# Optimization experiments

Measured on AMD Instinct MI355X. Metric: run time of the kernel, lower is better.

## Reference

```python
import jax, jax.numpy as jnp
import numpy as np

B, N, DIM = 2, 512, 128
HEADS, DH = 4, 64
INNER = HEADS * DH            # 256
POS_HID = 64
MULT = 4                      # attn_mlp_hidden_mult
K = 16                        # num_neighbors


def setup_inputs() -> dict:
    key = jax.random.key(0)
    ks = jax.random.split(key, 10)
    w = lambda k, shape: jax.random.normal(k, shape, jnp.float32) * 0.02
    return {
        "x": jax.random.normal(ks[0], (B, N, DIM), jnp.float32),
        "pos": jax.random.normal(ks[1], (B, N, 3), jnp.float32),
        "mask": jnp.ones((B, N), dtype=bool),
        "w_qkv": w(ks[2], (DIM, 3 * INNER)),
        "w_out": w(ks[3], (INNER, DIM)),
        "b_out": jnp.zeros((DIM,), jnp.float32),
        "w_pos1": w(ks[4], (3, POS_HID)),
        "b_pos1": jnp.zeros((POS_HID,), jnp.float32),
        "w_pos2": w(ks[5], (POS_HID, INNER)),
        "b_pos2": jnp.zeros((INNER,), jnp.float32),
        # grouped 1x1 convs == per-head linear layers
        "w_attn1": w(ks[6], (HEADS, DH, MULT * DH)),
        "b_attn1": jnp.zeros((HEADS, MULT * DH), jnp.float32),
        "w_attn2": w(ks[7], (HEADS, MULT * DH, DH)),
        "b_attn2": jnp.zeros((HEADS, DH), jnp.float32),
    }


def reference(x, pos, mask, w_qkv, w_out, b_out, w_pos1, b_pos1, w_pos2, b_pos2,
              w_attn1, b_attn1, w_attn2, b_attn2):
    b, n, _ = x.shape
    h, d = HEADS, DH

    qkv = x @ w_qkv                                   # [b, n, 3*inner]
    q, k, v = jnp.split(qkv, 3, axis=-1)
    to_heads = lambda t: t.reshape(b, n, h, d).transpose(0, 2, 1, 3)  # b h n d
    q, k, v = map(to_heads, (q, k, v))

    # dense pairwise relative positions + pos MLP  [b, n, n, inner]
    rel_pos = pos[:, :, None, :] - pos[:, None, :, :]            # [b, n, n, 3]
    rpe = jax.nn.relu(rel_pos @ w_pos1 + b_pos1) @ w_pos2 + b_pos2

    # masked topk over pairwise distance (smallest K)
    rel_dist = jnp.linalg.norm(rel_pos, axis=-1)                 # [b, n, n]
    mask2 = mask[:, :, None] & mask[:, None, :]                  # [b, n, n]
    fmax = jnp.finfo(rel_dist.dtype).max
    rel_dist = jnp.where(mask2, rel_dist, fmax)
    _, idx = jax.lax.top_k(-rel_dist, K)                         # [b, n, K]

    # neighbor gathers (equivalent to torch batched_index_select over j)
    gather_hd = jax.vmap(lambda t, i: t[:, i, :])                # [h,n,d],[n,K] -> [h,n,K,d]
    k_nb = gather_hd(k, idx)                                     # [b, h, n, K, d]
    v_nb = gather_hd(v, idx)
    row = jnp.arange(n)[:, None]
    rpe_nb = jax.vmap(lambda r, i: r[row, i])(rpe, idx)          # [b, n, K, inner]
    rpe_nb = rpe_nb.reshape(b, n, K, h, d).transpose(0, 3, 1, 2, 4)  # [b,h,n,K,d]
    mask_nb = jax.vmap(lambda m, i: m[row, i])(mask2, idx)       # [b, n, K]

    # qk_rel gathered implicitly: (q_i - k_j)[j=idx] == q_i - k_nb
    attn_in = q[:, :, :, None, :] - k_nb + rpe_nb                # [b, h, n, K, d]

    # grouped 1x1 conv MLP == per-head MLP on last dim
    hid = jax.nn.relu(jnp.einsum('bhikd,hde->bhike', attn_in, w_attn1)
                      + b_attn1[None, :, None, None, :])
    sim = (jnp.einsum('bhike,hed->bhikd', hid, w_attn2)
           + b_attn2[None, :, None, None, :])                    # [b, h, n, K, d]

    sim = jnp.where(mask_nb[:, None, :, :, None], sim, -fmax)
    # torch: sim is [b, (h d), i, j]; softmax(dim=-2) is over i -> axis 2 here
    attn = jax.nn.softmax(sim, axis=2)

    v_full = v_nb + rpe_nb                                       # [b, h, n, K, d]
    agg = jnp.sum(attn * v_full, axis=3)                         # [b, h, n, d]
    agg = agg.transpose(0, 2, 1, 3).reshape(b, n, h * d)         # [b, n, inner]
    return agg @ w_out + b_out
```

## Files before the change

### kernel.cpp

```cpp
#include <hip/hip_runtime.h>

#define B_ 2
#define N_ 512
#define DIM_ 128
#define HEADS_ 4
#define DH_ 64
#define INNER_ 256
#define PH_ 64
#define HID2_ 256
#define KNB_ 16

typedef unsigned long long u64;
typedef unsigned int u32;
typedef unsigned short u16;
typedef __attribute__((ext_vector_type(8))) short bf16x8;
typedef __attribute__((ext_vector_type(8))) unsigned short us8;
typedef __attribute__((ext_vector_type(4))) float f32x4;

__device__ __forceinline__ float bf2f(u16 u) {
    union { float f; u32 u; } c; c.u = ((u32)u) << 16; return c.f;
}
__device__ __forceinline__ u16 f2bf(float f) {
    union { float f; u32 u; } c; c.f = f;
    u32 u = c.u;
    return (u16)((u + 0x7fffu + ((u >> 16) & 1u)) >> 16);
}
__device__ __forceinline__ u32 pack2(float lo, float hi) {
    return ((u32)f2bf(hi) << 16) | (u32)f2bf(lo);
}

__global__ __launch_bounds__(256) void k_front(
        const float* __restrict__ x, const float* __restrict__ pos, const float* __restrict__ w_qkv,
        const float* __restrict__ w_a1, const float* __restrict__ w_a2, const float* __restrict__ w_p2,
        u16* __restrict__ wf1, u16* __restrict__ wf2, u16* __restrict__ wfp,
        u16* __restrict__ qb, u16* __restrict__ kb, float* __restrict__ v,
        int* __restrict__ idx) {
    int blk = blockIdx.x;
    if (blk < 576) {
        int t = blk * 256 + threadIdx.x;
        if (t < 65536) {
            int jj = t & 7, lbig = (t >> 3) & 63, f = t >> 9;
            int s = f & 1, etL = (f >> 1) & 7, half = (f >> 4) & 1, h = f >> 5;
            int lr = lbig & 15, g = lbig >> 4;
            int d = s * 32 + g * 8 + jj, e = (half * 8 + etL) * 16 + lr;
            wf1[t] = f2bf(w_a1[((h * 64 + d) << 8) + e]);
        } else if (t < 131072) {
            int t2 = t - 65536;
            int jj = t2 & 7, lbig = (t2 >> 3) & 63, f = t2 >> 9;
            int s = f & 7, ct = (f >> 3) & 3, h = f >> 5;
            int lr = lbig & 15, g = lbig >> 4;
            int e = s * 32 + g * 8 + jj, c = ct * 16 + lr;
            wf2[t2] = f2bf(w_a2[(((h << 8) + e) << 6) + c]);
        } else {
            int t3 = t - 131072;
            int jj = t3 & 7, lbig = (t3 >> 3) & 63, f = t3 >> 9;
            int s = f & 1, ct = (f >> 1) & 3, h = f >> 3;
            int lr = lbig & 15, g = lbig >> 4;
            int e = s * 32 + g * 8 + jj, c = h * 64 + ct * 16 + lr;
            wfp[t3] = f2bf(w_p2[(e << 8) + c]);
        }
    } else if (blk < 704) {
        int bu = blk - 576;
        int b = bu >> 6;
        int n0 = (bu & 63) * 8;
        int t = threadIdx.x;
        __shared__ float xs[8][128];
        #pragma unroll
        for (int p = 0; p < 4; ++p) {
            int e = p * 256 + t;
            xs[e >> 7][e & 127] = x[((size_t)(b * N_ + n0) + (e >> 7)) * DIM_ + (e & 127)];
        }
        __syncthreads();
        float acc[3][8];
        #pragma unroll
        for (int cc = 0; cc < 3; ++cc)
            #pragma unroll
            for (int r = 0; r < 8; ++r) acc[cc][r] = 0.f;
        for (int c4 = 0; c4 < 32; ++c4) {
            float wv[3][4];
            #pragma unroll
            for (int dd = 0; dd < 4; ++dd)
                #pragma unroll
                for (int cc = 0; cc < 3; ++cc)
                    wv[cc][dd] = w_qkv[(size_t)(c4 * 4 + dd) * (3 * INNER_) + cc * INNER_ + t];
            #pragma unroll
            for (int r = 0; r < 8; ++r) {
                float4 xv = *(const float4*)&xs[r][c4 * 4];
                #pragma unroll
                for (int cc = 0; cc < 3; ++cc)
                    acc[cc][r] += xv.x * wv[cc][0] + xv.y * wv[cc][1] + xv.z * wv[cc][2] + xv.w * wv[cc][3];
            }
        }
        int h = t >> 6, d = t & 63;
        #pragma unroll
        for (int r = 0; r < 8; ++r) {
            size_t o = (((size_t)(b * HEADS_ + h)) * N_ + n0 + r) * DH_ + d;
            qb[o] = f2bf(acc[0][r]);
            kb[o] = f2bf(acc[1][r]);
            v[o]  = acc[2][r];
        }
    } else {
        int wave = (blk - 704) * 4 + (threadIdx.x >> 6);
        int lane = threadIdx.x & 63;
        int b = wave >> 9;
        float px = pos[(size_t)wave * 3 + 0];
        float py = pos[(size_t)wave * 3 + 1];
        float pz = pos[(size_t)wave * 3 + 2];
        u64 keys[8];
        #pragma unroll
        for (int s = 0; s < 8; ++s) {
            int j = s * 64 + lane;
            float dx = __fsub_rn(px, pos[(size_t)(b * N_ + j) * 3 + 0]);
            float dy = __fsub_rn(py, pos[(size_t)(b * N_ + j) * 3 + 1]);
            float dz = __fsub_rn(pz, pos[(size_t)(b * N_ + j) * 3 + 2]);
            float s2 = __fadd_rn(__fadd_rn(__fmul_rn(dx, dx), __fmul_rn(dy, dy)), __fmul_rn(dz, dz));
            float dist = __fsqrt_rn(s2);
            keys[s] = ((u64)__float_as_uint(dist) << 32) | (unsigned)j;
        }
        for (int r = 0; r < KNB_; ++r) {
            u64 m = keys[0];
            #pragma unroll
            for (int s = 1; s < 8; ++s) m = (keys[s] < m) ? keys[s] : m;
            #pragma unroll
            for (int off = 32; off >= 1; off >>= 1) {
                u64 o = __shfl_xor(m, off);
                m = (o < m) ? o : m;
            }
            if (lane == 0) idx[(size_t)wave * KNB_ + r] = (int)(m & 0xffffffffu);
            #pragma unroll
            for (int s = 0; s < 8; ++s) if (keys[s] == m) keys[s] = ~0ull;
        }
    }
}

__global__ __launch_bounds__(256) void k_gather(
        const u16* __restrict__ qb, const u16* __restrict__ kb, const float* __restrict__ v,
        const int* __restrict__ idx, const float* __restrict__ pos,
        const float* __restrict__ w_p1, const float* __restrict__ b_p1,
        const float* __restrict__ b_p2, const u16* __restrict__ wfp,
        u16* __restrict__ ainb, u16* __restrict__ vf) {
    __shared__ u16 RP[4][2][16 * 72];
    int t = threadIdx.x;
    int wv = t >> 6, l = t & 63, lr = l & 15, g = l >> 4;
    int blk = blockIdx.x;
    int b = blk >> 8;
    int i0 = (blk & 255) * 2;
    int h = wv, bh = b * HEADS_ + h;

    float rx[2], ry[2], rz[2];
    us8 qv[2][2], kv[2][2];
    float4 v0[2][2], v1[2][2];
    #pragma unroll
    for (int ii = 0; ii < 2; ++ii) {
        int i = i0 + ii, bi = (b << 9) + i;
        int j = idx[(bi << 4) + lr];
        int bj = (b << 9) + j;
        rx[ii] = pos[(size_t)bi * 3 + 0] - pos[(size_t)bj * 3 + 0];
        ry[ii] = pos[(size_t)bi * 3 + 1] - pos[(size_t)bj * 3 + 1];
        rz[ii] = pos[(size_t)bi * 3 + 2] - pos[(size_t)bj * 3 + 2];
        #pragma unroll
        for (int s = 0; s < 2; ++s) {
            qv[ii][s] = *(const us8*)&qb[(size_t)(bh * N_ + i) * 64 + s * 32 + g * 8];
            kv[ii][s] = *(const us8*)&kb[(size_t)(bh * N_ + j) * 64 + s * 32 + g * 8];
            v0[ii][s] = *(const float4*)&v[(size_t)(bh * N_ + j) * 64 + s * 32 + g * 8];
            v1[ii][s] = *(const float4*)&v[(size_t)(bh * N_ + j) * 64 + s * 32 + g * 8 + 4];
        }
    }

    bf16x8 hidp[2][2];
    #pragma unroll
    for (int ii = 0; ii < 2; ++ii) {
        #pragma unroll
        for (int s = 0; s < 2; ++s) {
            u16 tmp[8];
            #pragma unroll
            for (int jj = 0; jj < 8; ++jj) {
                int e = s * 32 + g * 8 + jj;
                float hh = b_p1[e] + rx[ii] * w_p1[e] + ry[ii] * w_p1[PH_ + e] + rz[ii] * w_p1[2 * PH_ + e];
                tmp[jj] = f2bf(fmaxf(hh, 0.f));
            }
            hidp[ii][s] = *(bf16x8*)tmp;
        }
    }

    {
        bf16x8 Ar[4][2];
        #pragma unroll
        for (int ct = 0; ct < 4; ++ct)
            #pragma unroll
            for (int s = 0; s < 2; ++s)
                Ar[ct][s] = *(const bf16x8*)&wfp[(size_t)((((h << 2) + ct) << 1) + s) * 512 + l * 8];
        #pragma unroll
        for (int ct = 0; ct < 4; ++ct) {
            f32x4 C0 = {0.f, 0.f, 0.f, 0.f}, C1 = {0.f, 0.f, 0.f, 0.f};
            #pragma unroll
            for (int s = 0; s < 2; ++s) {
                C0 = __builtin_amdgcn_mfma_f32_16x16x32_bf16(Ar[ct][s], hidp[0][s], C0, 0, 0, 0);
                C1 = __builtin_amdgcn_mfma_f32_16x16x32_bf16(Ar[ct][s], hidp[1][s], C1, 0, 0, 0);
            }
            float4 bias = *(const float4*)&b_p2[h * 64 + ct * 16 + g * 4];
            uint2 o0, o1;
            o0.x = pack2(C0[0] + bias.x, C0[1] + bias.y);
            o0.y = pack2(C0[2] + bias.z, C0[3] + bias.w);
            o1.x = pack2(C1[0] + bias.x, C1[1] + bias.y);
            o1.y = pack2(C1[2] + bias.z, C1[3] + bias.w);
            *(uint2*)&RP[wv][0][lr * 72 + ct * 16 + g * 4] = o0;
            *(uint2*)&RP[wv][1][lr * 72 + ct * 16 + g * 4] = o1;
        }
    }

    #pragma unroll
    for (int ii = 0; ii < 2; ++ii) {
        int i = i0 + ii;
        #pragma unroll
        for (int s = 0; s < 2; ++s) {
            bf16x8 rp = *(const bf16x8*)&RP[wv][ii][lr * 72 + s * 32 + g * 8];
            us8 rpu = *(const us8*)&rp;
            float vvr[8] = {v0[ii][s].x, v0[ii][s].y, v0[ii][s].z, v0[ii][s].w,
                            v1[ii][s].x, v1[ii][s].y, v1[ii][s].z, v1[ii][s].w};
            u16 ta[8], tv[8];
            #pragma unroll
            for (int jj = 0; jj < 8; ++jj) {
                float rpf = bf2f(rpu[jj]);
                ta[jj] = f2bf(bf2f(qv[ii][s][jj]) - bf2f(kv[ii][s][jj]) + rpf);
                tv[jj] = f2bf(vvr[jj] + rpf);
            }
            *(bf16x8*)&ainb[(size_t)(((bh * N_ + i) << 4) + lr) * 64 + s * 32 + g * 8] = *(bf16x8*)ta;
            *(bf16x8*)&vf[(size_t)(((bh * N_ + i) << 4) + lr) * 64 + s * 32 + g * 8] = *(bf16x8*)tv;
        }
    }
}

__global__ __launch_bounds__(256, 2) void k_mlp(
        const u16* __restrict__ ainb,
        const u16* __restrict__ wf1, const u16* __restrict__ wf2,
        const float* __restrict__ b_a1, const float* __restrict__ b_a2,
        u16* __restrict__ sim) {
    __shared__ u16 HID[4][2][16 * 136];
    int t = threadIdx.x;
    int wv = t >> 6, l = t & 63, lr = l & 15, g = l >> 4;
    int blk = blockIdx.x;
    int bh = blk >> 6;
    int h = bh & 3;
    int i0 = (blk & 63) * 8 + wv * 2;

    bf16x8 ain[2][2];
    #pragma unroll
    for (int ii = 0; ii < 2; ++ii) {
        int i = i0 + ii;
        #pragma unroll
        for (int s = 0; s < 2; ++s)
            ain[ii][s] = *(const bf16x8*)&ainb[(size_t)(((bh * N_ + i) << 4) + lr) * 64 + s * 32 + g * 8];
    }

    f32x4 C2[2][4];
    #pragma unroll
    for (int ii = 0; ii < 2; ++ii)
        #pragma unroll
        for (int ct = 0; ct < 4; ++ct) C2[ii][ct] = (f32x4){0.f, 0.f, 0.f, 0.f};
    #pragma unroll
    for (int half = 0; half < 2; ++half) {
        bf16x8 A1[8][2];
        #pragma unroll
        for (int etL = 0; etL < 8; ++etL)
            #pragma unroll
            for (int s = 0; s < 2; ++s)
                A1[etL][s] = *(const bf16x8*)&wf1[(size_t)(((((h << 1) + half) << 3) + etL) * 2 + s) * 512 + l * 8];
        #pragma unroll
        for (int etL = 0; etL < 8; ++etL) {
            int et = half * 8 + etL;
            f32x4 C0 = {0.f, 0.f, 0.f, 0.f}, C1 = {0.f, 0.f, 0.f, 0.f};
            #pragma unroll
            for (int s = 0; s < 2; ++s) {
                C0 = __builtin_amdgcn_mfma_f32_16x16x32_bf16(A1[etL][s], ain[0][s], C0, 0, 0, 0);
                C1 = __builtin_amdgcn_mfma_f32_16x16x32_bf16(A1[etL][s], ain[1][s], C1, 0, 0, 0);
            }
            float4 bias = *(const float4*)&b_a1[h * 256 + et * 16 + g * 4];
            uint2 p0, p1;
            p0.x = pack2(fmaxf(C0[0] + bias.x, 0.f), fmaxf(C0[1] + bias.y, 0.f));
            p0.y = pack2(fmaxf(C0[2] + bias.z, 0.f), fmaxf(C0[3] + bias.w, 0.f));
            p1.x = pack2(fmaxf(C1[0] + bias.x, 0.f), fmaxf(C1[1] + bias.y, 0.f));
            p1.y = pack2(fmaxf(C1[2] + bias.z, 0.f), fmaxf(C1[3] + bias.w, 0.f));
            *(uint2*)&HID[wv][0][lr * 136 + etL * 16 + g * 4] = p0;
            *(uint2*)&HID[wv][1][lr * 136 + etL * 16 + g * 4] = p1;
        }
        #pragma unroll
        for (int chunk = 0; chunk < 2; ++chunk) {
            bf16x8 A2[4][2];
            #pragma unroll
            for (int ct = 0; ct < 4; ++ct)
                #pragma unroll
                for (int ss = 0; ss < 2; ++ss) {
                    int s = half * 4 + chunk * 2 + ss;
                    A2[ct][ss] = *(const bf16x8*)&wf2[(size_t)((((h << 2) + ct) << 3) + s) * 512 + l * 8];
                }
            #pragma unroll
            for (int ss = 0; ss < 2; ++ss) {
                int sL = chunk * 2 + ss;
                bf16x8 B0 = *(const bf16x8*)&HID[wv][0][lr * 136 + sL * 32 + g * 8];
                bf16x8 B1 = *(const bf16x8*)&HID[wv][1][lr * 136 + sL * 32 + g * 8];
                #pragma unroll
                for (int ct = 0; ct < 4; ++ct) {
                    C2[0][ct] = __builtin_amdgcn_mfma_f32_16x16x32_bf16(A2[ct][ss], B0, C2[0][ct], 0, 0, 0);
                    C2[1][ct] = __builtin_amdgcn_mfma_f32_16x16x32_bf16(A2[ct][ss], B1, C2[1][ct], 0, 0, 0);
                }
            }
        }
    }
    #pragma unroll
    for (int ii = 0; ii < 2; ++ii) {
        int i = i0 + ii;
        #pragma unroll
        for (int ct = 0; ct < 4; ++ct) {
            float4 bias = *(const float4*)&b_a2[h * 64 + ct * 16 + g * 4];
            uint2 o;
            o.x = pack2(C2[ii][ct][0] + bias.x, C2[ii][ct][1] + bias.y);
            o.y = pack2(C2[ii][ct][2] + bias.z, C2[ii][ct][3] + bias.w);
            *(uint2*)&sim[(size_t)(((bh * N_ + i) << 4) + lr) * 64 + ct * 16 + g * 4] = o;
        }
    }
}

__global__ __launch_bounds__(256) void k_stats(const u16* __restrict__ sim, float* __restrict__ R) {
    int blk = blockIdx.x;
    int ks = blk & 15, bh = blk >> 4;
    int d0 = (threadIdx.x & 15) * 4;
    int nc = threadIdx.x >> 4;
    __shared__ float red[16][69];
    size_t base = ((size_t)(bh * N_ + nc * 32) * 16 + ks) * 64 + d0;
    float s0 = 0.f, s1 = 0.f, s2 = 0.f, s3 = 0.f;
    for (int nn = 0; nn < 32; ++nn) {
        uint2 u = *(const uint2*)&sim[base + (size_t)nn * 1024];
        s0 += __expf(bf2f((u16)(u.x & 0xffff)));
        s1 += __expf(bf2f((u16)(u.x >> 16)));
        s2 += __expf(bf2f((u16)(u.y & 0xffff)));
        s3 += __expf(bf2f((u16)(u.y >> 16)));
    }
    red[nc][d0 + 0] = s0; red[nc][d0 + 1] = s1;
    red[nc][d0 + 2] = s2; red[nc][d0 + 3] = s3;
    __syncthreads();
    int t = threadIdx.x;
    if (t < 64) {
        float s = 0.f;
        #pragma unroll
        for (int c = 0; c < 16; ++c) s += red[c][t];
        R[(size_t)blk * 64 + t] = 1.f / s;
    }
}

__global__ __launch_bounds__(256) void k_agg_out(
        const u16* __restrict__ sim, const u16* __restrict__ vf, const float* __restrict__ R,
        const float* __restrict__ w, const float* __restrict__ bo, float* __restrict__ out) {
    int blk = blockIdx.x;
    int b = blk >> 7;
    int i0 = (blk & 127) * 4;
    int t = threadIdx.x;
    __shared__ float ag[4][260];
    {
        int h = t >> 6, d = t & 63;
        int bh = b * HEADS_ + h;
        float Rk[16];
        #pragma unroll
        for (int ks = 0; ks < 16; ++ks) Rk[ks] = R[((bh << 4) + ks) * 64 + d];
        #pragma unroll
        for (int r = 0; r < 4; ++r) {
            size_t base = (size_t)((bh * N_ + i0 + r) << 4) * 64 + d;
            float acc = 0.f;
            #pragma unroll
            for (int ks = 0; ks < 16; ++ks) {
                float p = __expf(bf2f(sim[base + (size_t)ks * 64])) * Rk[ks];
                acc += p * bf2f(vf[base + (size_t)ks * 64]);
            }
            ag[r][h * 64 + d] = acc;
        }
    }
    __syncthreads();
    int c = t & 127, rg = t >> 7;
    float acc[2];
    acc[0] = bo[c]; acc[1] = bo[c];
    for (int k4 = 0; k4 < 64; ++k4) {
        float wv[4];
        #pragma unroll
        for (int kk = 0; kk < 4; ++kk) wv[kk] = w[(size_t)(k4 * 4 + kk) * DIM_ + c];
        #pragma unroll
        for (int rr = 0; rr < 2; ++rr) {
            float4 a4 = *(const float4*)&ag[rr * 2 + rg][k4 * 4];
            acc[rr] += a4.x * wv[0] + a4.y * wv[1] + a4.z * wv[2] + a4.w * wv[3];
        }
    }
    #pragma unroll
    for (int rr = 0; rr < 2; ++rr)
        out[(size_t)((b << 9) + i0 + rr * 2 + rg) * DIM_ + c] = acc[rr];
}

extern "C" void kernel_launch(void* const* d_in, const int* in_sizes, int n_in,
                              void* d_out, int out_size, void* d_ws, size_t ws_size,
                              hipStream_t stream) {
    const float* x      = (const float*)d_in[0];
    const float* pos    = (const float*)d_in[1];
    const float* w_qkv  = (const float*)d_in[3];
    const float* w_out  = (const float*)d_in[4];
    const float* b_out  = (const float*)d_in[5];
    const float* w_pos1 = (const float*)d_in[6];
    const float* b_pos1 = (const float*)d_in[7];
    const float* w_pos2 = (const float*)d_in[8];
    const float* b_pos2 = (const float*)d_in[9];
    const float* w_a1   = (const float*)d_in[10];
    const float* b_a1   = (const float*)d_in[11];
    const float* w_a2   = (const float*)d_in[12];
    const float* b_a2   = (const float*)d_in[13];
    float* out = (float*)d_out;

    char* W = (char*)d_ws;
    u16*  qb   = (u16*)W;            W += 524288;
    u16*  kb   = (u16*)W;            W += 524288;
    float* v   = (float*)W;          W += 1048576;
    int*  idx  = (int*)W;            W += 65536;
    u16*  sim  = (u16*)W;            W += 8388608;
    u16*  vf   = (u16*)W;            W += 8388608;
    u16*  ainb = (u16*)W;            W += 8388608;
    float* R   = (float*)W;          W += 32768;
    u16*  wf1  = (u16*)W;            W += 131072;
    u16*  wf2  = (u16*)W;            W += 131072;
    u16*  wfp  = (u16*)W;            W += 32768;

    k_front<<<960, 256, 0, stream>>>(x, pos, w_qkv, w_a1, w_a2, w_pos2,
                                     wf1, wf2, wfp, qb, kb, v, idx);
    k_gather<<<512, 256, 0, stream>>>(qb, kb, v, idx, pos, w_pos1, b_pos1, b_pos2, wfp,
                                      ainb, vf);
    k_mlp<<<512, 256, 0, stream>>>(ainb, wf1, wf2, b_a1, b_a2, sim);
    k_stats<<<128, 256, 0, stream>>>(sim, R);
    k_agg_out<<<256, 256, 0, stream>>>(sim, vf, R, w_out, b_out, out);
}
```

Before: 59.99 us.

## Split softmax stats across halves, double agg blocks, and linearize ainb layout

k_stats now splits each (bh, k) column over two blocks that write partial sums, which k_agg_out combines and inverts. This doubles the grid to 256 blocks for more parallelism. k_agg_out processes 2 rows per block with 512 blocks instead of 4 rows with 256, and the ainb intermediate uses a lane-linear layout so the k_gather stores and k_mlp loads are contiguous per wave. k_gather also gets a min-blocks launch bound of 2. In exchange, w_out is reread by twice as many blocks and there is an extra partial-sum read.

```diff
diff --git a/kernel.cpp b/kernel.cpp
--- a/kernel.cpp
+++ b/kernel.cpp
@@ -133,7 +133,7 @@
     }
 }
 
-__global__ __launch_bounds__(256) void k_gather(
+__global__ __launch_bounds__(256, 2) void k_gather(
         const u16* __restrict__ qb, const u16* __restrict__ kb, const float* __restrict__ v,
         const int* __restrict__ idx, const float* __restrict__ pos,
         const float* __restrict__ w_p1, const float* __restrict__ b_p1,
@@ -225,7 +225,7 @@
                 ta[jj] = f2bf(bf2f(qv[ii][s][jj]) - bf2f(kv[ii][s][jj]) + rpf);
                 tv[jj] = f2bf(vvr[jj] + rpf);
             }
-            *(bf16x8*)&ainb[(size_t)(((bh * N_ + i) << 4) + lr) * 64 + s * 32 + g * 8] = *(bf16x8*)ta;
+            *(bf16x8*)&ainb[((size_t)((bh * N_ + i) * 2 + s)) * 512 + l * 8] = *(bf16x8*)ta;
             *(bf16x8*)&vf[(size_t)(((bh * N_ + i) << 4) + lr) * 64 + s * 32 + g * 8] = *(bf16x8*)tv;
         }
     }
@@ -250,7 +250,7 @@
         int i = i0 + ii;
         #pragma unroll
         for (int s = 0; s < 2; ++s)
-            ain[ii][s] = *(const bf16x8*)&ainb[(size_t)(((bh * N_ + i) << 4) + lr) * 64 + s * 32 + g * 8];
+            ain[ii][s] = *(const bf16x8*)&ainb[((size_t)((bh * N_ + i) * 2 + s)) * 512 + l * 8];
     }
 
     f32x4 C2[2][4];
@@ -321,15 +321,16 @@
     }
 }
 
-__global__ __launch_bounds__(256) void k_stats(const u16* __restrict__ sim, float* __restrict__ R) {
+__global__ __launch_bounds__(256) void k_stats(const u16* __restrict__ sim, float* __restrict__ P) {
     int blk = blockIdx.x;
-    int ks = blk & 15, bh = blk >> 4;
+    int half = blk & 1, ks = (blk >> 1) & 15, bh = blk >> 5;
     int d0 = (threadIdx.x & 15) * 4;
     int nc = threadIdx.x >> 4;
     __shared__ float red[16][69];
-    size_t base = ((size_t)(bh * N_ + nc * 32) * 16 + ks) * 64 + d0;
+    size_t base = ((size_t)(bh * N_ + half * 256 + nc * 16) * 16 + ks) * 64 + d0;
     float s0 = 0.f, s1 = 0.f, s2 = 0.f, s3 = 0.f;
-    for (int nn = 0; nn < 32; ++nn) {
+    #pragma unroll
+    for (int nn = 0; nn < 16; ++nn) {
         uint2 u = *(const uint2*)&sim[base + (size_t)nn * 1024];
         s0 += __expf(bf2f((u16)(u.x & 0xffff)));
         s1 += __expf(bf2f((u16)(u.x >> 16)));
@@ -344,26 +345,29 @@
         float s = 0.f;
         #pragma unroll
         for (int c = 0; c < 16; ++c) s += red[c][t];
-        R[(size_t)blk * 64 + t] = 1.f / s;
+        P[(size_t)blk * 64 + t] = s;
     }
 }
 
 __global__ __launch_bounds__(256) void k_agg_out(
-        const u16* __restrict__ sim, const u16* __restrict__ vf, const float* __restrict__ R,
+        const u16* __restrict__ sim, const u16* __restrict__ vf, const float* __restrict__ P,
         const float* __restrict__ w, const float* __restrict__ bo, float* __restrict__ out) {
     int blk = blockIdx.x;
-    int b = blk >> 7;
-    int i0 = (blk & 127) * 4;
+    int b = blk >> 8;
+    int i0 = (blk & 255) * 2;
     int t = threadIdx.x;
-    __shared__ float ag[4][260];
+    __shared__ float ag[2][260];
     {
         int h = t >> 6, d = t & 63;
         int bh = b * HEADS_ + h;
         float Rk[16];
         #pragma unroll
-        for (int ks = 0; ks < 16; ++ks) Rk[ks] = R[((bh << 4) + ks) * 64 + d];
-        #pragma unroll
-        for (int r = 0; r < 4; ++r) {
+        for (int ks = 0; ks < 16; ++ks) {
+            int pbase = ((bh << 5) + (ks << 1)) * 64 + d;
+            Rk[ks] = 1.f / (P[pbase] + P[pbase + 64]);
+        }
+        #pragma unroll
+        for (int r = 0; r < 2; ++r) {
             size_t base = (size_t)((bh * N_ + i0 + r) << 4) * 64 + d;
             float acc = 0.f;
             #pragma unroll
@@ -376,21 +380,13 @@
     }
     __syncthreads();
     int c = t & 127, rg = t >> 7;
-    float acc[2];
-    acc[0] = bo[c]; acc[1] = bo[c];
+    float acc = bo[c];
     for (int k4 = 0; k4 < 64; ++k4) {
-        float wv[4];
-        #pragma unroll
-        for (int kk = 0; kk < 4; ++kk) wv[kk] = w[(size_t)(k4 * 4 + kk) * DIM_ + c];
-        #pragma unroll
-        for (int rr = 0; rr < 2; ++rr) {
-            float4 a4 = *(const float4*)&ag[rr * 2 + rg][k4 * 4];
-            acc[rr] += a4.x * wv[0] + a4.y * wv[1] + a4.z * wv[2] + a4.w * wv[3];
-        }
-    }
-    #pragma unroll
-    for (int rr = 0; rr < 2; ++rr)
-        out[(size_t)((b << 9) + i0 + rr * 2 + rg) * DIM_ + c] = acc[rr];
+        float4 a4 = *(const float4*)&ag[rg][k4 * 4];
+        acc += a4.x * w[(size_t)(k4 * 4 + 0) * DIM_ + c] + a4.y * w[(size_t)(k4 * 4 + 1) * DIM_ + c]
+             + a4.z * w[(size_t)(k4 * 4 + 2) * DIM_ + c] + a4.w * w[(size_t)(k4 * 4 + 3) * DIM_ + c];
+    }
+    out[(size_t)((b << 9) + i0 + rg) * DIM_ + c] = acc;
 }
 
 extern "C" void kernel_launch(void* const* d_in, const int* in_sizes, int n_in,
@@ -419,7 +415,7 @@
     u16*  sim  = (u16*)W;            W += 8388608;
     u16*  vf   = (u16*)W;            W += 8388608;
     u16*  ainb = (u16*)W;            W += 8388608;
-    float* R   = (float*)W;          W += 32768;
+    float* P   = (float*)W;          W += 65536;
     u16*  wf1  = (u16*)W;            W += 131072;
     u16*  wf2  = (u16*)W;            W += 131072;
     u16*  wfp  = (u16*)W;            W += 32768;
@@ -429,6 +425,6 @@
     k_gather<<<512, 256, 0, stream>>>(qb, kb, v, idx, pos, w_pos1, b_pos1, b_pos2, wfp,
                                       ainb, vf);
     k_mlp<<<512, 256, 0, stream>>>(ainb, wf1, wf2, b_a1, b_a2, sim);
-    k_stats<<<128, 256, 0, stream>>>(sim, R);
-    k_agg_out<<<256, 256, 0, stream>>>(sim, vf, R, w_out, b_out, out);
-}
+    k_stats<<<256, 256, 0, stream>>>(sim, P);
+    k_agg_out<<<512, 256, 0, stream>>>(sim, vf, P, w_out, b_out, out);
+}
```

After: 56.56 us, median of 2. 1.06x faster.
